# Kernel optimization log

Measured on AMD Instinct MI355X. Metric: run time of the kernel, lower is better.

Reference implementation:

```python
import jax, jax.numpy as jnp
import numpy as np

B, N = 2, 6
FC, FH, FW = 256, 32, 88            # encoder feature shape
ORFH, ORFW = 256, 704               # original image H, W
OUT_C = 128
D_ST, D_END, D_STEP = 1.0, 60.0, 3.0
NXV, NYV, NZV = 256, 256, 1         # BEV voxel grid (x, y, z)
DXV = np.array([0.4, 0.4, 20.0], np.float32)          # dx
BXV = np.array([-51.0, -51.0, 0.0], np.float32)       # bx = bound_lo + dx/2
BN_EPS = 1e-3


def _conv(x, w, b):
    y = jax.lax.conv_general_dilated(x, w, (1, 1), 'SAME',
                                     dimension_numbers=('NCHW', 'OIHW', 'NCHW'))
    return y + b[None, :, None, None]


def _bn(x, scale, bias, mean, var):
    inv = scale / jnp.sqrt(var + BN_EPS)
    return x * inv[None, :, None, None] + (bias - mean * inv)[None, :, None, None]


def _frustum():
    ds = jnp.arange(D_ST, D_END, D_STEP, dtype=jnp.float32)      # (D,)
    xs = jnp.linspace(0.0, ORFW - 1.0, FW)
    ys = jnp.linspace(0.0, ORFH - 1.0, FH)
    f = jnp.stack(jnp.broadcast_arrays(xs[None, None, :], ys[None, :, None],
                                       ds[:, None, None]), axis=-1)  # (D,FH,FW,3)
    return f, ds


def _forward(cam2ego_rot, cam2ego_trans, cam_intrins, post_cam2ego_rot,
             post_cam2ego_trans, img_feats,
             conv1_w, conv1_b, bn1_s, bn1_b, bn1_m, bn1_v,
             conv2_w, conv2_b, bn2_s, bn2_b, bn2_m, bn2_v,
             conv3_w, conv3_b):
    frustum, depth_vals = _frustum()
    D = depth_vals.shape[0]
    # ---- geometry (GaussianLSS.get_geometry) ----
    pts = frustum[None, None] - post_cam2ego_trans[:, :, None, None, None, :]
    inv_post = jnp.linalg.inv(post_cam2ego_rot)                       # (B,N,3,3)
    pts = jnp.einsum('bnij,bndhwj->bndhwi', inv_post, pts)
    pts = jnp.concatenate([pts[..., :2] * pts[..., 2:3], pts[..., 2:3]], -1)
    combine = cam2ego_rot @ jnp.linalg.inv(cam_intrins)
    geometry = (jnp.einsum('bnij,bndhwj->bndhwi', combine, pts)
                + cam2ego_trans[:, :, None, None, None, :])           # (B,N,D,H,W,3)
    # ---- depth net + gaussian depth distribution (get_cam_feature) ----
    x = img_feats.reshape(B * N, FC, FH, FW)
    x = jax.nn.relu(_bn(_conv(x, conv1_w, conv1_b), bn1_s, bn1_b, bn1_m, bn1_v))
    x = jax.nn.relu(_bn(_conv(x, conv2_w, conv2_b), bn2_s, bn2_b, bn2_m, bn2_v))
    x = _conv(x, conv3_w, conv3_b)                                    # (BN, OUT_C+2, H, W)
    mu, log_sigma, feats = x[:, 0], x[:, 1], x[:, 2:]
    sigma = jnp.exp(log_sigma) + 1e-6
    g = jnp.exp(-0.5 * (depth_vals[None, :, None, None] - mu[:, None]) ** 2
                / (sigma[:, None] ** 2))                              # (BN,D,H,W)
    g = g / (jnp.sum(g, axis=1, keepdims=True) + 1e-6)
    vol = g[:, None] * feats[:, :, None]                              # (BN,C,D,H,W)
    vol = vol.reshape(B, N, OUT_C, D, FH, FW).transpose(0, 1, 3, 4, 5, 2)  # (B,N,D,H,W,C)
    # ---- bev_pool: voxelize + scatter-add ----
    dx = jnp.asarray(DXV)
    bx = jnp.asarray(BXV)
    geom = ((geometry - (bx - dx / 2.0)) / dx).astype(jnp.int32)      # trunc like .long()
    gx, gy, gz = geom[..., 0], geom[..., 1], geom[..., 2]
    kept = ((gx >= 0) & (gx < NXV) & (gy >= 0) & (gy < NYV)
            & (gz >= 0) & (gz < NZV))                                 # (B,N,D,H,W)
    bidx = jnp.arange(B, dtype=jnp.int32)[:, None, None, None, None]
    flat = ((bidx * NZV + gz) * NXV + gx) * NYV + gy
    flat = jnp.where(kept, flat, 0)
    w = kept.astype(vol.dtype)
    data = (vol * w[..., None]).reshape(-1, OUT_C)
    bev = jax.ops.segment_sum(data, flat.reshape(-1),
                              num_segments=B * NZV * NXV * NYV)
    # torch: (B,C,Z,X,Y) -> cat(unbind(dim=2), 1) -> (B, Z*C, X, Y)
    bev = bev.reshape(B, NZV, NXV, NYV, OUT_C).transpose(0, 1, 4, 2, 3)
    bev = bev.reshape(B, NZV * OUT_C, NXV, NYV)
    # ---- ref_bev_pool mask ----
    counts = jax.ops.segment_sum(w.reshape(-1), flat.reshape(-1),
                                 num_segments=B * NZV * NXV * NYV)
    mask = jnp.any(counts.reshape(B, NZV, NXV, NYV) > 0, axis=1)      # (B,X,Y) bool
    return bev, mask


def setup_inputs() -> dict:
    key = jax.random.key(0)
    ks = jax.random.split(key, 16)
    # camera->ego rotation: cam z -> ego x, cam x -> -ego y, cam y -> -ego z
    R = jnp.array([[0., 0., 1.], [-1., 0., 0.], [0., -1., 0.]], jnp.float32)
    cam2ego_rot = jnp.tile(R, (B, N, 1, 1)) + 0.01 * jax.random.normal(ks[0], (B, N, 3, 3))
    cam2ego_trans = jax.random.uniform(ks[1], (B, N, 3), minval=-2.0, maxval=2.0)
    K = jnp.array([[500., 0., ORFW / 2.], [0., 500., ORFH / 2.], [0., 0., 1.]], jnp.float32)
    cam_intrins = jnp.tile(K, (B, N, 1, 1))
    post_cam2ego_rot = jnp.tile(jnp.eye(3, dtype=jnp.float32), (B, N, 1, 1)) \
        + 0.005 * jax.random.normal(ks[2], (B, N, 3, 3))
    post_cam2ego_trans = 0.5 * jax.random.normal(ks[3], (B, N, 3))
    img_feats = 0.1 * jax.random.normal(ks[4], (B, N, FC, FH, FW))
    conv3_b = jnp.zeros((OUT_C + 2,)).at[0].set(25.0).at[1].set(2.3)  # mu~25m, sigma~10m
    return dict(
        cam2ego_rot=cam2ego_rot, cam2ego_trans=cam2ego_trans,
        cam_intrins=cam_intrins, post_cam2ego_rot=post_cam2ego_rot,
        post_cam2ego_trans=post_cam2ego_trans, img_feats=img_feats,
        conv1_w=0.02 * jax.random.normal(ks[5], (FC, FC, 3, 3)),
        conv1_b=jnp.zeros((FC,)),
        bn1_s=1.0 + 0.01 * jax.random.normal(ks[6], (FC,)),
        bn1_b=0.01 * jax.random.normal(ks[7], (FC,)),
        bn1_m=0.01 * jax.random.normal(ks[8], (FC,)),
        bn1_v=1.0 + 0.1 * jax.random.uniform(ks[9], (FC,)),
        conv2_w=0.02 * jax.random.normal(ks[10], (FC, FC, 3, 3)),
        conv2_b=jnp.zeros((FC,)),
        bn2_s=1.0 + 0.01 * jax.random.normal(ks[11], (FC,)),
        bn2_b=0.01 * jax.random.normal(ks[12], (FC,)),
        bn2_m=0.01 * jax.random.normal(ks[13], (FC,)),
        bn2_v=1.0 + 0.1 * jax.random.uniform(ks[14], (FC,)),
        conv3_w=0.02 * jax.random.normal(ks[15], (OUT_C + 2, FC, 1, 1)),
        conv3_b=conv3_b,
    )


def reference(cam2ego_rot, cam2ego_trans, cam_intrins, post_cam2ego_rot,
              post_cam2ego_trans, img_feats,
              conv1_w, conv1_b, bn1_s, bn1_b, bn1_m, bn1_v,
              conv2_w, conv2_b, bn2_s, bn2_b, bn2_m, bn2_v,
              conv3_w, conv3_b):
    return _forward(cam2ego_rot, cam2ego_trans, cam_intrins, post_cam2ego_rot,
                    post_cam2ego_trans, img_feats,
                    conv1_w, conv1_b, bn1_s, bn1_b, bn1_m, bn1_v,
                    conv2_w, conv2_b, bn2_s, bn2_b, bn2_m, bn2_v,
                    conv3_w, conv3_b)
```

## Files before the change

kernel.cpp:

```cpp
#include <hip/hip_runtime.h>
#include <math.h>

typedef unsigned short ushort_t;
typedef unsigned int uint_t;

#define NIMG 12
#define NCH  256
#define FH   32
#define FW   88
#define NPIX 2816
#define NDEP 20
#define NOUTC 128
#define NVOX 65536
#define NPTS 675840
#define NKEY 131072
#define BEV_FLOATS 16777216u

#define B_MATS   0u
#define B_A1     4096u
#define B_C1     5120u
#define B_A2     6144u
#define B_C2     7168u
#define B_TOT    278528u
#define B_FEAT   282624u
#define B_RECS   17584128u
#define B_BEV    22990848u
#define B_VCODE  22990848u
#define B_WT     25694208u
#define B_CNT    28397568u
#define B_OFFS   28921856u
#define B_CUR    29446144u
#define B_SPINE  29970432u
#define B_XBF    29972480u
#define B_ACT1   47273984u
#define B_ACT2   64575488u
#define B_WSWZ1  81876992u
#define B_WSWZ2  83056640u
#define B_WSWZ3  84236288u

typedef __attribute__((ext_vector_type(8))) short bf16x8;
typedef __attribute__((ext_vector_type(4))) float floatx4;
typedef __attribute__((ext_vector_type(4))) uint_t u32x4;

__device__ __forceinline__ ushort_t f2bf(float f) {
    uint_t x = __float_as_uint(f);
    return (ushort_t)((x + 0x7fffu + ((x >> 16) & 1u)) >> 16);
}
__device__ __forceinline__ float bf2f(ushort_t u) {
    return __uint_as_float(((uint_t)u) << 16);
}

__device__ __forceinline__ void inv3x3(const float* __restrict__ M, float* __restrict__ o) {
    float a=M[0],b=M[1],c=M[2],d=M[3],e=M[4],f=M[5],g=M[6],h=M[7],i=M[8];
    float A = e*i - f*h;
    float B = c*h - b*i;
    float C = b*f - c*e;
    float D = f*g - d*i;
    float E = a*i - c*g;
    float F = c*d - a*f;
    float G = d*h - e*g;
    float H = b*g - a*h;
    float I = a*e - b*d;
    float det = a*A + b*D + c*G;
    float id = 1.0f / det;
    o[0]=A*id; o[1]=B*id; o[2]=C*id;
    o[3]=D*id; o[4]=E*id; o[5]=F*id;
    o[6]=G*id; o[7]=H*id; o[8]=I*id;
}

__device__ __forceinline__ void wprep_one(
    const float* __restrict__ w, ushort_t* __restrict__ dst,
    int ntap, int ncib, int ncog, int nco, int nci, int idx, bool split)
{
    int j = idx & 7;
    int l = (idx >> 3) & 63;
    int pairidx = idx >> 9;
    int g = pairidx % ncog;
    int b = (pairidx / ncog) % ncib;
    int t = pairidx / (ncog * ncib);
    int co = g * 16 + (l & 15);
    int ci = b * 32 + (l >> 4) * 8 + j;
    float v = 0.0f;
    if (co < nco) v = w[((size_t)co * nci + ci) * ntap + t];
    ushort_t hi = f2bf(v);
    if (split) {
        dst[(size_t)pairidx * 1024 + l * 8 + j]       = hi;
        dst[(size_t)pairidx * 1024 + 512 + l * 8 + j] = f2bf(v - bf2f(hi));
    } else {
        dst[(size_t)pairidx * 512 + l * 8 + j] = hi;
    }
}

__global__ __launch_bounds__(256) void wprep_all_kernel(
    const float* __restrict__ w1, ushort_t* __restrict__ d1,
    const float* __restrict__ w2, ushort_t* __restrict__ d2,
    const float* __restrict__ w3, ushort_t* __restrict__ d3,
    const float* __restrict__ c2e_rot, const float* __restrict__ c2e_trans,
    const float* __restrict__ intrins, const float* __restrict__ post_rot,
    const float* __restrict__ post_trans,
    const float* __restrict__ c1b, const float* __restrict__ s1,
    const float* __restrict__ bb1, const float* __restrict__ m1, const float* __restrict__ v1,
    const float* __restrict__ c2b, const float* __restrict__ s2,
    const float* __restrict__ bb2, const float* __restrict__ m2, const float* __restrict__ v2,
    float* __restrict__ mats, float* __restrict__ A1, float* __restrict__ C1,
    float* __restrict__ A2, float* __restrict__ C2)
{
    int bid = blockIdx.x;
    int t = threadIdx.x;
    if (bid < 2304) {
        wprep_one(w1, d1, 9, 8, 16, 256, 256, bid * 256 + t, false);
    } else if (bid < 4608) {
        wprep_one(w2, d2, 9, 8, 16, 256, 256, (bid - 2304) * 256 + t, false);
    } else if (bid < 4752) {
        int idx = (bid - 4608) * 256 + t;
        if (idx < 36864) wprep_one(w3, d3, 1, 8, 9, 130, 256, idx, true);
    } else {
        if (t < NIMG) {
            float ip[9], ki[9], comb[9];
            inv3x3(post_rot + t*9, ip);
            inv3x3(intrins  + t*9, ki);
            const float* R = c2e_rot + t*9;
            #pragma unroll
            for (int r = 0; r < 3; ++r)
                #pragma unroll
                for (int c = 0; c < 3; ++c)
                    comb[r*3+c] = R[r*3+0]*ki[0*3+c] + R[r*3+1]*ki[1*3+c] + R[r*3+2]*ki[2*3+c];
            float* M = mats + t*24;
            #pragma unroll
            for (int k = 0; k < 9; ++k) { M[k] = ip[k]; M[9+k] = comb[k]; }
            M[18] = c2e_trans[t*3+0]; M[19] = c2e_trans[t*3+1]; M[20] = c2e_trans[t*3+2];
            M[21] = post_trans[t*3+0]; M[22] = post_trans[t*3+1]; M[23] = post_trans[t*3+2];
        }
        float i1 = s1[t] / sqrtf(v1[t] + 1e-3f);
        A1[t] = i1;
        C1[t] = (c1b[t] - m1[t]) * i1 + bb1[t];
        float i2 = s2[t] / sqrtf(v2[t] + 1e-3f);
        A2[t] = i2;
        C2[t] = (c2b[t] - m2[t]) * i2 + bb2[t];
    }
}

__global__ __launch_bounds__(256) void geom_kernel(
    const float* __restrict__ mats, int* __restrict__ vcode, uint_t* __restrict__ cnt)
{
    int i = blockIdx.x * 256 + threadIdx.x;
    int lane = threadIdx.x & 63;
    int hw  = i % NPIX;
    int tmp = i / NPIX;
    int d   = tmp % NDEP;
    int bn  = tmp / NDEP;
    int h = hw / FW, w = hw - h * FW;
    const float* M = mats + bn * 24;
    float xs = (float)w * (703.0f / 87.0f);
    float ys = (float)h * (255.0f / 31.0f);
    float dv = 1.0f + 3.0f * (float)d;
    float fx = xs - M[21], fy = ys - M[22], fz = dv - M[23];
    float p0 = M[0]*fx + M[1]*fy + M[2]*fz;
    float p1 = M[3]*fx + M[4]*fy + M[5]*fz;
    float p2 = M[6]*fx + M[7]*fy + M[8]*fz;
    p0 *= p2; p1 *= p2;
    float gx = M[ 9]*p0 + M[10]*p1 + M[11]*p2 + M[18];
    float gy = M[12]*p0 + M[13]*p1 + M[14]*p2 + M[19];
    float gz = M[15]*p0 + M[16]*p1 + M[17]*p2 + M[20];
    const float cx = -51.0f - 0.2f, cy = -51.0f - 0.2f, cz = 0.0f - 10.0f;
    int ix = (int)((gx - cx) / 0.4f);
    int iy = (int)((gy - cy) / 0.4f);
    int iz = (int)((gz - cz) / 20.0f);
    bool kept = (ix >= 0) && (ix < 256) && (iy >= 0) && (iy < 256) && (iz == 0);
    int code = kept ? ((ix << 8) | iy) : -1;
    vcode[i] = code;

    int b = bn / 6;
    uint_t key = kept ? (uint_t)((b << 16) | code) : 0xFFFFFFFFu;
    uint_t prevkey = __shfl_up(key, 1);
    bool leader = (lane == 0) || (key != prevkey);
    unsigned long long mask = __ballot(leader);
    if (leader && kept) {
        unsigned long long higher = mask & ~((2ULL << lane) - 1ULL);
        int nxt = higher ? (__ffsll((long long)higher) - 1) : 64;
        atomicAdd(&cnt[key], (uint_t)(nxt - lane));
    }
}

__global__ __launch_bounds__(256) void cast_transpose_kernel(
    const float* __restrict__ in, ushort_t* __restrict__ out)
{
    __shared__ __align__(16) ushort_t lds[64 * 264];
    int img = blockIdx.y;
    int px0 = blockIdx.x * 64;
    int t = threadIdx.x;
    const float* src = in + (size_t)img * NCH * NPIX;
    int pxl = t & 63;
    int cib = t >> 6;
    #pragma unroll 4
    for (int cc = 0; cc < 64; ++cc) {
        int ci = cc * 4 + cib;
        float v = src[(size_t)ci * NPIX + px0 + pxl];
        lds[pxl * 264 + ci] = f2bf(v);
    }
    __syncthreads();
    int wv = t >> 6, lane = t & 63;
    uint2* outv = (uint2*)out;
    #pragma unroll
    for (int i = 0; i < 16; ++i) {
        int p = wv * 16 + i;
        uint2 val = *(const uint2*)&lds[p * 264 + lane * 4];
        outv[(size_t)(img * NPIX + px0 + p) * 64 + lane] = val;
    }
}

__global__ __launch_bounds__(256, 3) void conv3x3_mfma(
    const ushort_t* __restrict__ in,
    const ushort_t* __restrict__ wswz,
    const float* __restrict__ Abn, const float* __restrict__ Cbn,
    ushort_t* __restrict__ out)
{
    __shared__ __align__(16) ushort_t lds[2][8640];
    int bx = blockIdx.x;
    int cg = blockIdx.y;
    int img = bx >> 5, h = bx & 31;
    int t = threadIdx.x;
    int w = t >> 6, l = t & 63;
    int q = l >> 4, c = l & 15;
    const int n0s[6] = {0, 16, 32, 48, 64, 72};

    for (int i = t; i < 8640; i += 256) ((uint_t*)lds)[i] = 0;

    const u32x4* src4 = (const u32x4*)(in + (size_t)img * NPIX * 256);
    const bf16x8* wsA = (const bf16x8*)wswz;

    int gbase[5], loff[5];
    bool sval[5];
    #pragma unroll
    for (int k = 0; k < 5; ++k) {
        int p = t + k * 256;
        bool valid = (p < 1056);
        int chunk = p >> 2, sub = p & 3;
        int r = chunk / 88;
        int col = chunk - r * 88;
        int hin = h - 1 + r;
        bool inb = valid && (hin >= 0) && (hin < FH);
        sval[k] = inb;
        gbase[k] = inb ? ((hin * 88 + col) * 32 + sub) : 0;
        int cs = col + 1;
        int slot = sub ^ ((cs >> 1) & 3);
        loff[k] = ((r * 90 + cs) * 4 + slot) * 8;
    }

    floatx4 acc[2][6];
    #pragma unroll
    for (int m = 0; m < 2; ++m)
        #pragma unroll
        for (int n = 0; n < 6; ++n)
            acc[m][n] = (floatx4){0.f, 0.f, 0.f, 0.f};

    int g0 = cg * 8 + w * 2;

    __syncthreads();
    #pragma unroll
    for (int k = 0; k < 5; ++k)
        if (sval[k]) *(u32x4*)&lds[0][loff[k]] = src4[gbase[k]];

    int buf = 0;
    for (int kb = 0; kb < 8; ++kb) {
        __syncthreads();
        u32x4 sreg[5];
        if (kb < 7) {
            #pragma unroll
            for (int k = 0; k < 5; ++k)
                if (sval[k]) sreg[k] = src4[gbase[k] + (kb + 1) * 4];
        }
        const bf16x8* B = (const bf16x8*)lds[buf];

        bf16x8 a0, a1;
        {
            int pa = (0 * 8 + kb) * 16;
            a0 = wsA[(size_t)(pa + g0    ) * 64 + l];
            a1 = wsA[(size_t)(pa + g0 + 1) * 64 + l];
        }
        #pragma unroll
        for (int t9 = 0; t9 < 9; ++t9) {
            bf16x8 na0, na1;
            if (t9 < 8) {
                int pa = ((t9 + 1) * 8 + kb) * 16;
                na0 = wsA[(size_t)(pa + g0    ) * 64 + l];
                na1 = wsA[(size_t)(pa + g0 + 1) * 64 + l];
            }
            int ky = t9 / 3, kx = t9 - ky * 3;
            #pragma unroll
            for (int n = 0; n < 6; ++n) {
                int col = n0s[n] + kx + c;
                int slot = q ^ ((col >> 1) & 3);
                bf16x8 b = B[(ky * 90 + col) * 4 + slot];
                acc[0][n] = __builtin_amdgcn_mfma_f32_16x16x32_bf16(a0, b, acc[0][n], 0, 0, 0);
                acc[1][n] = __builtin_amdgcn_mfma_f32_16x16x32_bf16(a1, b, acc[1][n], 0, 0, 0);
            }
            if (t9 < 8) { a0 = na0; a1 = na1; }
        }
        if (kb < 7) {
            #pragma unroll
            for (int k = 0; k < 5; ++k)
                if (sval[k]) *(u32x4*)&lds[buf ^ 1][loff[k]] = sreg[k];
        }
        buf ^= 1;
    }

    #pragma unroll
    for (int m = 0; m < 2; ++m) {
        int cob = cg * 128 + w * 32 + m * 16 + q * 4;
        float ba0 = Abn[cob+0], ba1 = Abn[cob+1], ba2 = Abn[cob+2], ba3 = Abn[cob+3];
        float bc0 = Cbn[cob+0], bc1 = Cbn[cob+1], bc2 = Cbn[cob+2], bc3 = Cbn[cob+3];
        #pragma unroll
        for (int n = 0; n < 6; ++n) {
            if (n == 5 && c < 8) continue;
            int col = n0s[n] + c;
            floatx4 v = acc[m][n];
            uint_t lo = (uint_t)f2bf(fmaxf(v[0]*ba0+bc0, 0.f)) | ((uint_t)f2bf(fmaxf(v[1]*ba1+bc1, 0.f)) << 16);
            uint_t hi = (uint_t)f2bf(fmaxf(v[2]*ba2+bc2, 0.f)) | ((uint_t)f2bf(fmaxf(v[3]*ba3+bc3, 0.f)) << 16);
            uint2 val; val.x = lo; val.y = hi;
            *(uint2*)&out[((size_t)img * NPIX + h * 88 + col) * 256 + cob] = val;
        }
    }
}

__global__ __launch_bounds__(256, 4) void gemm1x1_mfma(
    const ushort_t* __restrict__ act2,
    const ushort_t* __restrict__ wswz3,
    const float* __restrict__ b3,
    ushort_t* __restrict__ feat, float* __restrict__ wt)
{
    int t = threadIdx.x, wv = t >> 6, l = t & 63, q = l >> 4, c = l & 15;
    int n0 = (blockIdx.x * 4 + wv) * 16;
    int px = n0 + c;
    const bf16x8* A = (const bf16x8*)wswz3;
    const bf16x8* B = (const bf16x8*)act2;
    floatx4 acc[9];
    #pragma unroll
    for (int g = 0; g < 9; ++g) acc[g] = (floatx4){0.f, 0.f, 0.f, 0.f};
    for (int kb = 0; kb < 8; ++kb) {
        bf16x8 b = B[(size_t)px * 32 + kb * 4 + q];
        #pragma unroll
        for (int g = 0; g < 9; ++g) {
            size_t pa = (size_t)(kb * 9 + g) * 128;
            acc[g] = __builtin_amdgcn_mfma_f32_16x16x32_bf16(A[pa + l],      b, acc[g], 0, 0, 0);
            acc[g] = __builtin_amdgcn_mfma_f32_16x16x32_bf16(A[pa + 64 + l], b, acc[g], 0, 0, 0);
        }
    }
    #pragma unroll
    for (int g = 0; g < 9; ++g) {
        #pragma unroll
        for (int r = 0; r < 4; ++r) {
            int co = g * 16 + q * 4 + r;
            if (co < 2 || co >= 130) continue;
            feat[(size_t)px * 128 + (co - 2)] = f2bf(acc[g][r] + b3[co]);
        }
    }
    float muv = acc[0][0] + b3[0];
    float lsv = acc[0][1] + b3[1];
    float mu_b  = __shfl(muv, c);
    float sig   = expf(__shfl(lsv, c)) + 1e-6f;
    float ninv2 = -0.5f / (sig * sig);
    float g5[5]; float s = 0.0f;
    #pragma unroll
    for (int j = 0; j < 5; ++j) {
        float dv = 1.0f + 3.0f * (float)(q * 5 + j);
        float df = dv - mu_b;
        g5[j] = expf(df * df * ninv2);
        s += g5[j];
    }
    s += __shfl_xor(s, 16);
    s += __shfl_xor(s, 32);
    float inv = 1.0f / (s + 1e-6f);
    #pragma unroll
    for (int j = 0; j < 5; ++j)
        wt[(size_t)px * NDEP + q * 5 + j] = g5[j] * inv;
}

__global__ __launch_bounds__(256) void scan_block_kernel(
    const uint_t* __restrict__ cnt, uint_t* __restrict__ offs, uint_t* __restrict__ spine)
{
    __shared__ uint_t s[256];
    int t = threadIdx.x;
    int i = blockIdx.x * 256 + t;
    uint_t v = cnt[i];
    s[t] = v;
    __syncthreads();
    #pragma unroll
    for (int off = 1; off < 256; off <<= 1) {
        uint_t add = (t >= off) ? s[t - off] : 0u;
        __syncthreads();
        s[t] += add;
        __syncthreads();
    }
    offs[i] = s[t] - v;
    if (t == 255) spine[blockIdx.x] = s[255];
}

__global__ __launch_bounds__(256) void fixup_kernel(
    uint_t* __restrict__ offs, const uint_t* __restrict__ spine,
    uint_t* __restrict__ cursor, const uint_t* __restrict__ cnt,
    float* __restrict__ mask_out, uint_t* __restrict__ total)
{
    __shared__ uint_t red[256];
    int bid = blockIdx.x, t = threadIdx.x;
    uint_t part = 0;
    for (int j = t; j < bid; j += 256) part += spine[j];
    red[t] = part;
    __syncthreads();
    #pragma unroll
    for (int off = 128; off > 0; off >>= 1) {
        if (t < off) red[t] += red[t + off];
        __syncthreads();
    }
    uint_t prefix = red[0];
    int i = bid * 256 + t;
    uint_t o = offs[i] + prefix;
    offs[i] = o;
    cursor[i] = o;
    uint_t n = cnt[i];
    mask_out[i] = (n > 0) ? 1.0f : 0.0f;
    if (i == NKEY - 1) *total = o + n;
}

__global__ __launch_bounds__(256) void scatter_kernel(
    const int* __restrict__ vcode, const float* __restrict__ wt,
    uint_t* __restrict__ cursor, uint2* __restrict__ recs)
{
    int i = blockIdx.x * 256 + threadIdx.x;
    int lane = threadIdx.x & 63;
    int code = vcode[i];
    int hw  = i % NPIX;
    int tmp = i / NPIX;
    int d   = tmp % NDEP;
    int bn  = tmp / NDEP;
    int b   = bn / 6;
    int gp  = bn * NPIX + hw;
    bool active = (code >= 0);
    uint_t key = active ? (uint_t)((b << 16) | code) : 0xFFFFFFFFu;
    uint2 r;
    r.x = ((uint_t)(code & 0xffff) << 16) | (uint_t)gp;
    r.y = active ? __float_as_uint(wt[(size_t)gp * NDEP + d]) : 0u;

    uint_t prevkey = __shfl_up(key, 1);
    bool leader = (lane == 0) || (key != prevkey);
    unsigned long long mask = __ballot(leader);
    uint_t base = 0;
    if (leader && active) {
        unsigned long long higher = mask & ~((2ULL << lane) - 1ULL);
        int nxt = higher ? (__ffsll((long long)higher) - 1) : 64;
        base = atomicAdd(&cursor[key], (uint_t)(nxt - lane));
    }
    unsigned long long lower = mask & ((2ULL << lane) - 1ULL);
    int lead = 63 - __clzll((long long)lower);
    base = __shfl(base, lead);
    if (active) recs[base + (lane - lead)] = r;
}

__global__ __launch_bounds__(256) void segreduce_kernel(
    const uint2* __restrict__ recs, const uint_t* __restrict__ total,
    const uint_t* __restrict__ featu,
    float* __restrict__ bev_tmp)
{
    uint_t R = *total;
    int wid = blockIdx.x * 4 + (threadIdx.x >> 6);
    uint_t start = (uint_t)wid * 64u;
    if (start >= R) return;
    int lane = threadIdx.x & 63;
    uint_t ustart = __builtin_amdgcn_readfirstlane(start);

    uint2 r0 = recs[ustart];
    uint_t gp0 = r0.x & 0xffffu;
    uint_t prevk = ((gp0 >= 16896u) ? 0x10000u : 0u) | (r0.x >> 16);
    float acc0 = 0.f, acc1 = 0.f;

    #pragma unroll 8
    for (int e = 0; e < 64; ++e) {
        uint2 re = recs[ustart + e];
        uint_t gp = re.x & 0xffffu;
        uint_t key = ((gp >= 16896u) ? 0x10000u : 0u) | (re.x >> 16);
        float wv = __uint_as_float(re.y);
        if (ustart + e >= R) { key = prevk; wv = 0.f; gp = 0u; }
        if (key != prevk) {
            float* p = bev_tmp + (size_t)prevk * NOUTC;
            atomicAdd(p + 2 * lane,     acc0);
            atomicAdd(p + 2 * lane + 1, acc1);
            acc0 = acc1 = 0.f;
            prevk = key;
        }
        uint_t fv = featu[(size_t)gp * 64 + lane];
        acc0 = fmaf(wv, bf2f((ushort_t)(fv & 0xffffu)), acc0);
        acc1 = fmaf(wv, bf2f((ushort_t)(fv >> 16)),     acc1);
    }
    float* p = bev_tmp + (size_t)prevk * NOUTC;
    atomicAdd(p + 2 * lane,     acc0);
    atomicAdd(p + 2 * lane + 1, acc1);
}

__global__ __launch_bounds__(256) void transpose_kernel(
    const float* __restrict__ bev_tmp, float* __restrict__ bev_out)
{
    __shared__ float lds[64 * 129];
    int blk = blockIdx.x;
    int b   = blk >> 10;
    int v0  = (blk & 1023) * 64;
    int t   = threadIdx.x;
    const float* src = bev_tmp + ((size_t)b * NVOX + v0) * NOUTC;
    #pragma unroll
    for (int k = 0; k < 32; ++k) {
        int idx = k * 256 + t;
        int v = idx >> 7, ch = idx & 127;
        lds[v * 129 + ch] = src[idx];
    }
    __syncthreads();
    float* dst = bev_out + (size_t)b * NOUTC * NVOX + v0;
    #pragma unroll
    for (int k = 0; k < 32; ++k) {
        int idx = k * 256 + t;
        int vl = idx & 63, ch = idx >> 6;
        dst[(size_t)ch * NVOX + vl] = lds[vl * 129 + ch];
    }
}

extern "C" void kernel_launch(void* const* d_in, const int* in_sizes, int n_in,
                              void* d_out, int out_size, void* d_ws, size_t ws_size,
                              hipStream_t stream) {
    const float* c2e_rot    = (const float*)d_in[0];
    const float* c2e_trans  = (const float*)d_in[1];
    const float* intrins    = (const float*)d_in[2];
    const float* post_rot   = (const float*)d_in[3];
    const float* post_trans = (const float*)d_in[4];
    const float* img_feats  = (const float*)d_in[5];
    const float* conv1_w    = (const float*)d_in[6];
    const float* conv1_b    = (const float*)d_in[7];
    const float* bn1_s = (const float*)d_in[8];
    const float* bn1_b = (const float*)d_in[9];
    const float* bn1_m = (const float*)d_in[10];
    const float* bn1_v = (const float*)d_in[11];
    const float* conv2_w = (const float*)d_in[12];
    const float* conv2_b = (const float*)d_in[13];
    const float* bn2_s = (const float*)d_in[14];
    const float* bn2_b = (const float*)d_in[15];
    const float* bn2_m = (const float*)d_in[16];
    const float* bn2_v = (const float*)d_in[17];
    const float* conv3_w = (const float*)d_in[18];
    const float* conv3_b = (const float*)d_in[19];

    char* base = (char*)d_ws;
    float*    mats   = (float*)(base + B_MATS);
    float*    A1     = (float*)(base + B_A1);
    float*    C1     = (float*)(base + B_C1);
    float*    A2     = (float*)(base + B_A2);
    float*    C2     = (float*)(base + B_C2);
    uint_t*   total  = (uint_t*)(base + B_TOT);
    ushort_t* feat   = (ushort_t*)(base + B_FEAT);
    uint2*    recs   = (uint2*)(base + B_RECS);
    float*    bevtmp = (float*)(base + B_BEV);
    int*      vcode  = (int*)(base + B_VCODE);
    float*    wt     = (float*)(base + B_WT);
    uint_t*   cnt    = (uint_t*)(base + B_CNT);
    uint_t*   offs   = (uint_t*)(base + B_OFFS);
    uint_t*   cursor = (uint_t*)(base + B_CUR);
    uint_t*   spine  = (uint_t*)(base + B_SPINE);
    ushort_t* xbf    = (ushort_t*)(base + B_XBF);
    ushort_t* act1   = (ushort_t*)(base + B_ACT1);
    ushort_t* act2   = (ushort_t*)(base + B_ACT2);
    ushort_t* wswz1  = (ushort_t*)(base + B_WSWZ1);
    ushort_t* wswz2  = (ushort_t*)(base + B_WSWZ2);
    ushort_t* wswz3  = (ushort_t*)(base + B_WSWZ3);

    float* bev_out  = (float*)d_out;
    float* mask_out = bev_out + BEV_FLOATS;

    hipMemsetAsync(cnt, 0, NKEY * sizeof(uint_t), stream);
    wprep_all_kernel<<<4753, 256, 0, stream>>>(conv1_w, wswz1, conv2_w, wswz2, conv3_w, wswz3,
                                               c2e_rot, c2e_trans, intrins, post_rot, post_trans,
                                               conv1_b, bn1_s, bn1_b, bn1_m, bn1_v,
                                               conv2_b, bn2_s, bn2_b, bn2_m, bn2_v,
                                               mats, A1, C1, A2, C2);
    geom_kernel<<<NPTS / 256, 256, 0, stream>>>(mats, vcode, cnt);
    cast_transpose_kernel<<<dim3(44, 12), 256, 0, stream>>>(img_feats, xbf);
    conv3x3_mfma<<<dim3(NIMG * 32, 2), 256, 0, stream>>>(xbf,  wswz1, A1, C1, act1);
    conv3x3_mfma<<<dim3(NIMG * 32, 2), 256, 0, stream>>>(act1, wswz2, A2, C2, act2);
    gemm1x1_mfma<<<528, 256, 0, stream>>>(act2, wswz3, conv3_b, feat, wt);
    scan_block_kernel<<<NKEY / 256, 256, 0, stream>>>(cnt, offs, spine);
    fixup_kernel<<<NKEY / 256, 256, 0, stream>>>(offs, spine, cursor, cnt, mask_out, total);
    scatter_kernel<<<NPTS / 256, 256, 0, stream>>>(vcode, wt, cursor, recs);
    hipMemsetAsync(bevtmp, 0, (size_t)BEV_FLOATS * sizeof(float), stream);
    segreduce_kernel<<<(NPTS / 64 + 3) / 4, 256, 0, stream>>>(recs, total, (const uint_t*)feat, bevtmp);
    transpose_kernel<<<2048, 256, 0, stream>>>(bevtmp, bev_out);
}
```

Baseline: 378.9 us.

## Retile conv3x3 warps to 4x3 MFMA blocks and prefetch features in segreduce

```diff
diff --git a/kernel.cpp b/kernel.cpp
--- a/kernel.cpp
+++ b/kernel.cpp
@@ -222,7 +222,12 @@
     int t = threadIdx.x;
     int w = t >> 6, l = t & 63;
     int q = l >> 4, c = l & 15;
-    const int n0s[6] = {0, 16, 32, 48, 64, 72};
+    int cosub = w & 1, pxsub = w >> 1;
+
+    int myn0[3];
+    myn0[0] = pxsub ? 48 : 0;
+    myn0[1] = pxsub ? 64 : 16;
+    myn0[2] = pxsub ? 72 : 32;
 
     for (int i = t; i < 8640; i += 256) ((uint_t*)lds)[i] = 0;
 
@@ -247,14 +252,14 @@
         loff[k] = ((r * 90 + cs) * 4 + slot) * 8;
     }
 
-    floatx4 acc[2][6];
-    #pragma unroll
-    for (int m = 0; m < 2; ++m)
+    floatx4 acc[4][3];
+    #pragma unroll
+    for (int m = 0; m < 4; ++m)
         #pragma unroll
-        for (int n = 0; n < 6; ++n)
+        for (int n = 0; n < 3; ++n)
             acc[m][n] = (floatx4){0.f, 0.f, 0.f, 0.f};
 
-    int g0 = cg * 8 + w * 2;
+    int g0 = cg * 8 + cosub * 4;
 
     __syncthreads();
     #pragma unroll
@@ -272,30 +277,36 @@
         }
         const bf16x8* B = (const bf16x8*)lds[buf];
 
-        bf16x8 a0, a1;
+        bf16x8 a[4];
         {
             int pa = (0 * 8 + kb) * 16;
-            a0 = wsA[(size_t)(pa + g0    ) * 64 + l];
-            a1 = wsA[(size_t)(pa + g0 + 1) * 64 + l];
+            #pragma unroll
+            for (int m = 0; m < 4; ++m)
+                a[m] = wsA[(size_t)(pa + g0 + m) * 64 + l];
         }
         #pragma unroll
         for (int t9 = 0; t9 < 9; ++t9) {
-            bf16x8 na0, na1;
+            bf16x8 na[4];
             if (t9 < 8) {
                 int pa = ((t9 + 1) * 8 + kb) * 16;
-                na0 = wsA[(size_t)(pa + g0    ) * 64 + l];
-                na1 = wsA[(size_t)(pa + g0 + 1) * 64 + l];
+                #pragma unroll
+                for (int m = 0; m < 4; ++m)
+                    na[m] = wsA[(size_t)(pa + g0 + m) * 64 + l];
             }
             int ky = t9 / 3, kx = t9 - ky * 3;
             #pragma unroll
-            for (int n = 0; n < 6; ++n) {
-                int col = n0s[n] + kx + c;
+            for (int n = 0; n < 3; ++n) {
+                int col = myn0[n] + kx + c;
                 int slot = q ^ ((col >> 1) & 3);
                 bf16x8 b = B[(ky * 90 + col) * 4 + slot];
-                acc[0][n] = __builtin_amdgcn_mfma_f32_16x16x32_bf16(a0, b, acc[0][n], 0, 0, 0);
-                acc[1][n] = __builtin_amdgcn_mfma_f32_16x16x32_bf16(a1, b, acc[1][n], 0, 0, 0);
+                #pragma unroll
+                for (int m = 0; m < 4; ++m)
+                    acc[m][n] = __builtin_amdgcn_mfma_f32_16x16x32_bf16(a[m], b, acc[m][n], 0, 0, 0);
             }
-            if (t9 < 8) { a0 = na0; a1 = na1; }
+            if (t9 < 8) {
+                #pragma unroll
+                for (int m = 0; m < 4; ++m) a[m] = na[m];
+            }
         }
         if (kb < 7) {
             #pragma unroll
@@ -306,14 +317,14 @@
     }
 
     #pragma unroll
-    for (int m = 0; m < 2; ++m) {
-        int cob = cg * 128 + w * 32 + m * 16 + q * 4;
+    for (int m = 0; m < 4; ++m) {
+        int cob = cg * 128 + cosub * 64 + m * 16 + q * 4;
         float ba0 = Abn[cob+0], ba1 = Abn[cob+1], ba2 = Abn[cob+2], ba3 = Abn[cob+3];
         float bc0 = Cbn[cob+0], bc1 = Cbn[cob+1], bc2 = Cbn[cob+2], bc3 = Cbn[cob+3];
         #pragma unroll
-        for (int n = 0; n < 6; ++n) {
-            if (n == 5 && c < 8) continue;
-            int col = n0s[n] + c;
+        for (int n = 0; n < 3; ++n) {
+            if (pxsub == 1 && n == 2 && c < 8) continue;
+            int col = myn0[n] + c;
             floatx4 v = acc[m][n];
             uint_t lo = (uint_t)f2bf(fmaxf(v[0]*ba0+bc0, 0.f)) | ((uint_t)f2bf(fmaxf(v[1]*ba1+bc1, 0.f)) << 16);
             uint_t hi = (uint_t)f2bf(fmaxf(v[2]*ba2+bc2, 0.f)) | ((uint_t)f2bf(fmaxf(v[3]*ba3+bc3, 0.f)) << 16);
@@ -468,28 +479,50 @@
     int lane = threadIdx.x & 63;
     uint_t ustart = __builtin_amdgcn_readfirstlane(start);
 
-    uint2 r0 = recs[ustart];
-    uint_t gp0 = r0.x & 0xffffu;
-    uint_t prevk = ((gp0 >= 16896u) ? 0x10000u : 0u) | (r0.x >> 16);
+    uint_t myidx = ustart + (uint_t)lane;
+    if (myidx >= R) myidx = R - 1u;
+    uint2 mr = recs[myidx];
+
+    uint_t rx0 = (uint_t)__shfl((int)mr.x, 0);
+    uint_t gp00 = rx0 & 0xffffu;
+    uint_t prevk = ((gp00 >= 16896u) ? 0x10000u : 0u) | (rx0 >> 16);
     float acc0 = 0.f, acc1 = 0.f;
 
-    #pragma unroll 8
-    for (int e = 0; e < 64; ++e) {
-        uint2 re = recs[ustart + e];
-        uint_t gp = re.x & 0xffffu;
-        uint_t key = ((gp >= 16896u) ? 0x10000u : 0u) | (re.x >> 16);
-        float wv = __uint_as_float(re.y);
-        if (ustart + e >= R) { key = prevk; wv = 0.f; gp = 0u; }
-        if (key != prevk) {
-            float* p = bev_tmp + (size_t)prevk * NOUTC;
-            atomicAdd(p + 2 * lane,     acc0);
-            atomicAdd(p + 2 * lane + 1, acc1);
-            acc0 = acc1 = 0.f;
-            prevk = key;
-        }
-        uint_t fv = featu[(size_t)gp * 64 + lane];
-        acc0 = fmaf(wv, bf2f((ushort_t)(fv & 0xffffu)), acc0);
-        acc1 = fmaf(wv, bf2f((ushort_t)(fv >> 16)),     acc1);
+    uint_t fbuf[2][16];
+    #pragma unroll
+    for (int j = 0; j < 16; ++j) {
+        uint_t rx = (uint_t)__shfl((int)mr.x, j);
+        fbuf[0][j] = featu[(size_t)(rx & 0xffffu) * 64 + lane];
+    }
+    #pragma unroll
+    for (int b = 0; b < 4; ++b) {
+        if (b < 3) {
+            #pragma unroll
+            for (int j = 0; j < 16; ++j) {
+                uint_t rx = (uint_t)__shfl((int)mr.x, (b + 1) * 16 + j);
+                fbuf[(b + 1) & 1][j] = featu[(size_t)(rx & 0xffffu) * 64 + lane];
+            }
+        }
+        #pragma unroll
+        for (int j = 0; j < 16; ++j) {
+            int e = b * 16 + j;
+            uint_t rx = (uint_t)__shfl((int)mr.x, e);
+            uint_t ry = (uint_t)__shfl((int)mr.y, e);
+            uint_t gp = rx & 0xffffu;
+            uint_t key = ((gp >= 16896u) ? 0x10000u : 0u) | (rx >> 16);
+            float wv = __uint_as_float(ry);
+            if (ustart + (uint_t)e >= R) { key = prevk; wv = 0.f; }
+            if (key != prevk) {
+                float* p = bev_tmp + (size_t)prevk * NOUTC;
+                atomicAdd(p + 2 * lane,     acc0);
+                atomicAdd(p + 2 * lane + 1, acc1);
+                acc0 = acc1 = 0.f;
+                prevk = key;
+            }
+            uint_t fv = fbuf[b & 1][j];
+            acc0 = fmaf(wv, bf2f((ushort_t)(fv & 0xffffu)), acc0);
+            acc1 = fmaf(wv, bf2f((ushort_t)(fv >> 16)),     acc1);
+        }
     }
     float* p = bev_tmp + (size_t)prevk * NOUTC;
     atomicAdd(p + 2 * lane,     acc0);
```

Measured after the change: 369.9 us. 1.02x faster.
